# Kernel optimization log

Hardware: AMD Instinct MI355X
Metric: run time of the kernel (lower is better)

## Reference

```python
import jax, jax.numpy as jnp
import numpy as np
import math

B, S, D, H = 2, 2048, 768, 12
HD = D // H


def setup_inputs() -> dict:
    key = jax.random.key(0)
    ks = jax.random.split(key, 9)
    scale = 1.0 / math.sqrt(D)
    x = jax.random.normal(ks[0], (B, S, D), dtype=jnp.float32)
    # causal mask: True where attention is allowed (query i attends to key j<=i)
    mask = jnp.tril(jnp.ones((S, S), dtype=bool))[None, None]  # [1,1,S,S]
    wq = jax.random.normal(ks[1], (D, D), dtype=jnp.float32) * scale
    bq = jnp.zeros((D,), dtype=jnp.float32)
    wk = jax.random.normal(ks[2], (D, D), dtype=jnp.float32) * scale
    bk = jnp.zeros((D,), dtype=jnp.float32)
    wv = jax.random.normal(ks[3], (D, D), dtype=jnp.float32) * scale
    bv = jnp.zeros((D,), dtype=jnp.float32)
    wo = jax.random.normal(ks[4], (D, D), dtype=jnp.float32) * scale
    bo = jnp.zeros((D,), dtype=jnp.float32)
    return {"x": x, "mask": mask, "wq": wq, "bq": bq, "wk": wk, "bk": bk,
            "wv": wv, "bv": bv, "wo": wo, "bo": bo}


def reference(x, mask, wq, bq, wk, bk, wv, bv, wo, bo):
    b, s, d = x.shape
    # projections (flax Linear: y = x @ kernel + bias)
    q = (x @ wq + bq).reshape(b, s, H, HD).transpose(0, 2, 1, 3)  # [b,h,s,hd]
    k = (x @ wk + bk).reshape(b, s, H, HD).transpose(0, 2, 1, 3)
    v = (x @ wv + bv).reshape(b, s, H, HD).transpose(0, 2, 1, 3)
    scores = jnp.einsum('bhqd,bhkd->bhqk', q, k) / math.sqrt(HD)  # [b,h,s,s]
    scores = jnp.where(mask, scores, -jnp.inf)
    attn = jax.nn.softmax(scores, axis=-1)
    out = jnp.einsum('bhqk,bhkd->bhqd', attn, v)  # [b,h,s,hd]
    out = out.transpose(0, 2, 1, 3).reshape(b, s, d)
    return out @ wo + bo
```

## Files before the change

kernel.cpp:

```cpp
#include <hip/hip_runtime.h>
#include <math.h>

#define BATCH 2
#define SEQ   2048
#define DMODEL 768
#define NHEAD 12
#define HDIM  64

typedef unsigned short u16;
typedef __attribute__((ext_vector_type(8))) short bf16x8;
typedef __attribute__((ext_vector_type(4))) float f32x4;
typedef __attribute__((ext_vector_type(8))) unsigned short us8;
typedef __attribute__((ext_vector_type(4))) unsigned short us4;

__device__ __forceinline__ u16 f2bf(float f) {
    union { float f; unsigned u; } v; v.f = f;
    unsigned u = v.u;
    u += 0x7fff + ((u >> 16) & 1);
    return (u16)(u >> 16);
}

__device__ __forceinline__ u16 f2bf_trunc(float f) {
    union { float f; unsigned u; } v; v.f = f;
    return (u16)(v.u >> 16);
}

__device__ __forceinline__ float fexp2(float x) {
#if __has_builtin(__builtin_amdgcn_exp2f)
    return __builtin_amdgcn_exp2f(x);
#else
    return exp2f(x);
#endif
}

__device__ __forceinline__ void g2l16(const void* g, void* l) {
    __builtin_amdgcn_global_load_lds(
        (const __attribute__((address_space(1))) unsigned int*)g,
        (__attribute__((address_space(3))) unsigned int*)(unsigned int)(unsigned long long)(uintptr_t)l,
        16, 0, 0);
}

__device__ __forceinline__ void stage_rows(const u16* g, u16* lds, int nrows,
                                           int tid) {
    const int row = tid >> 2, col = (tid & 3) * 8;
    g2l16(g + (size_t)row * DMODEL + col, lds + tid * 8);
    if (nrows == 128) {
        g2l16(g + (size_t)(row + 64) * DMODEL + col, lds + 2048 + tid * 8);
    } else if (nrows == 96) {
        if (tid < 128)
            g2l16(g + (size_t)(row + 64) * DMODEL + col, lds + 2048 + tid * 8);
    }
}

__global__ __launch_bounds__(256) void prep(const float* __restrict__ x,
                                            const float* __restrict__ w0,
                                            const float* __restrict__ w1,
                                            const float* __restrict__ w2,
                                            const float* __restrict__ w3,
                                            u16* __restrict__ xb,
                                            u16* __restrict__ Wt_all) {
    __shared__ float t[32][33];
    const int bid = blockIdx.x;
    if (bid < 3072) {
        int i = bid * 256 + threadIdx.x;
        float4 v = ((const float4*)x)[i];
        us4 o;
        o.x = f2bf(v.x); o.y = f2bf(v.y); o.z = f2bf(v.z); o.w = f2bf(v.w);
        *(us4*)&xb[(size_t)i * 4] = o;
    } else {
        const int wid = bid - 3072;
        const int z  = wid / 576;
        const int rr = wid % 576;
        const int by = rr / 24, bx = rr % 24;
        const float* W = z == 0 ? w0 : z == 1 ? w1 : z == 2 ? w2 : w3;
        u16* Wt = Wt_all + (size_t)z * DMODEL * DMODEL;

        int tx = threadIdx.x & 31, ty = threadIdx.x >> 5;
        int xg = bx * 32 + tx;
        #pragma unroll
        for (int j = 0; j < 32; j += 8)
            t[ty + j][tx] = W[(size_t)(by * 32 + ty + j) * DMODEL + xg];
        __syncthreads();
        int x2 = by * 32 + tx;
        #pragma unroll
        for (int j = 0; j < 32; j += 8)
            Wt[(size_t)(bx * 32 + ty + j) * DMODEL + x2] = f2bf(t[tx][ty + j]);
    }
}

__global__ __launch_bounds__(256) void gemm_qkv(
    const u16* __restrict__ xb, const u16* __restrict__ WtQK,
    const u16* __restrict__ WtV,
    const float* __restrict__ bq, const float* __restrict__ bk,
    const float* __restrict__ bv,
    u16* __restrict__ QK, u16* __restrict__ Vt) {

    __shared__ __align__(16) u16 As[128 * 32];
    __shared__ __align__(16) u16 Bs[128 * 32];

    const int tid  = threadIdx.x;
    const int lane = tid & 63;
    const int w    = tid >> 6;
    const int quad = lane >> 4, l16 = lane & 15;
    const int wm   = w >> 1, wn = w & 1;
    const int b    = blockIdx.x;

    if (b < 512) {
        const int m0 = (b >> 4) * 128;
        const int n0 = (b & 15) * 96;
        f32x4 acc[4][3] = {};
        for (int k0 = 0; k0 < DMODEL; k0 += 32) {
            stage_rows(xb   + (size_t)m0 * DMODEL + k0, As, 128, tid);
            stage_rows(WtQK + (size_t)n0 * DMODEL + k0, Bs,  96, tid);
            __syncthreads();
            bf16x8 af[4], bfr[3];
            #pragma unroll
            for (int i = 0; i < 4; ++i)
                af[i] = *(const bf16x8*)&As[(wm * 64 + i * 16 + l16) * 32 + quad * 8];
            #pragma unroll
            for (int j = 0; j < 3; ++j)
                bfr[j] = *(const bf16x8*)&Bs[(wn * 48 + j * 16 + l16) * 32 + quad * 8];
            #pragma unroll
            for (int i = 0; i < 4; ++i)
                #pragma unroll
                for (int j = 0; j < 3; ++j)
                    acc[i][j] = __builtin_amdgcn_mfma_f32_16x16x32_bf16(af[i], bfr[j], acc[i][j], 0, 0, 0);
            __syncthreads();
        }
        const size_t n_elem = (size_t)BATCH * SEQ * DMODEL;
        #pragma unroll
        for (int j = 0; j < 3; ++j) {
            const int n     = n0 + wn * 48 + j * 16 + l16;
            const int which = n / 768;
            const int nn    = n - which * 768;
            const float bias  = (which == 0 ? bq : bk)[nn];
            const float scale = (which == 0) ? 0.18033688011112043f : 1.0f;
            const int h = nn >> 6, hd = nn & 63;
            u16* outw = QK + (size_t)which * n_elem;
            #pragma unroll
            for (int i = 0; i < 4; ++i) {
                const int mbase = m0 + wm * 64 + i * 16 + quad * 4;
                #pragma unroll
                for (int r = 0; r < 4; ++r) {
                    const int m  = mbase + r;
                    const int b_ = m >> 11, s_ = m & 2047;
                    outw[(size_t)((b_ * NHEAD + h) * SEQ + s_) * HDIM + hd] =
                        f2bf((acc[i][j][r] + bias) * scale);
                }
            }
        }
    } else {
        const int vj = b - 512;
        const int m0 = (vj & 7) * 96;
        const int n0 = (vj >> 3) * 128;
        f32x4 acc[3][4] = {};
        for (int k0 = 0; k0 < DMODEL; k0 += 32) {
            stage_rows(WtV + (size_t)m0 * DMODEL + k0, As,  96, tid);
            stage_rows(xb  + (size_t)n0 * DMODEL + k0, Bs, 128, tid);
            __syncthreads();
            bf16x8 af[3], bfr[4];
            #pragma unroll
            for (int i = 0; i < 3; ++i)
                af[i] = *(const bf16x8*)&As[(wm * 48 + i * 16 + l16) * 32 + quad * 8];
            #pragma unroll
            for (int j = 0; j < 4; ++j)
                bfr[j] = *(const bf16x8*)&Bs[(wn * 64 + j * 16 + l16) * 32 + quad * 8];
            #pragma unroll
            for (int i = 0; i < 3; ++i)
                #pragma unroll
                for (int j = 0; j < 4; ++j)
                    acc[i][j] = __builtin_amdgcn_mfma_f32_16x16x32_bf16(af[i], bfr[j], acc[i][j], 0, 0, 0);
            __syncthreads();
        }
        #pragma unroll
        for (int i = 0; i < 3; ++i) {
            const int rbase = m0 + wm * 48 + i * 16 + quad * 4;
            #pragma unroll
            for (int r = 0; r < 4; ++r) {
                const int row_g = rbase + r;
                const float bias = bv[row_g];
                const int h = row_g >> 6, hd = row_g & 63;
                #pragma unroll
                for (int j = 0; j < 4; ++j) {
                    const int col_g = n0 + wn * 64 + j * 16 + l16;
                    const int b_ = col_g >> 11, s_ = col_g & 2047;
                    Vt[(size_t)((b_ * NHEAD + h) * HDIM + hd) * SEQ + s_] =
                        f2bf(acc[i][j][r] + bias);
                }
            }
        }
    }
}

__global__ __launch_bounds__(256) void gemm_out(
    const u16* __restrict__ Ag, const u16* __restrict__ Bt,
    const float* __restrict__ bo, float* __restrict__ out) {

    __shared__ __align__(16) u16 As[64 * 32];
    __shared__ __align__(16) u16 Bs[64 * 32];

    const int tid  = threadIdx.x;
    const int lane = tid & 63;
    const int w    = tid >> 6;
    const int quad = lane >> 4, l16 = lane & 15;
    const int wm   = w >> 1, wn = w & 1;
    const int m0 = blockIdx.x * 64, n0 = blockIdx.y * 64;

    const int rowA = tid >> 2;
    const int kch  = (tid & 3) * 8;

    f32x4 acc[2][2] = {};

    for (int k0 = 0; k0 < DMODEL; k0 += 32) {
        g2l16(Ag + (size_t)(m0 + rowA) * DMODEL + k0 + kch, As + tid * 8);
        g2l16(Bt + (size_t)(n0 + rowA) * DMODEL + k0 + kch, Bs + tid * 8);
        __syncthreads();

        bf16x8 af[2], bfr[2];
        #pragma unroll
        for (int i = 0; i < 2; ++i)
            af[i] = *(const bf16x8*)&As[(wm * 32 + i * 16 + l16) * 32 + quad * 8];
        #pragma unroll
        for (int j = 0; j < 2; ++j)
            bfr[j] = *(const bf16x8*)&Bs[(wn * 32 + j * 16 + l16) * 32 + quad * 8];
        #pragma unroll
        for (int i = 0; i < 2; ++i)
            #pragma unroll
            for (int j = 0; j < 2; ++j)
                acc[i][j] = __builtin_amdgcn_mfma_f32_16x16x32_bf16(af[i], bfr[j], acc[i][j], 0, 0, 0);
        __syncthreads();
    }

    #pragma unroll
    for (int i = 0; i < 2; ++i) {
        const int mbase = m0 + wm * 32 + i * 16 + quad * 4;
        #pragma unroll
        for (int r = 0; r < 4; ++r) {
            const int m = mbase + r;
            #pragma unroll
            for (int j = 0; j < 2; ++j) {
                const int n = n0 + wn * 32 + j * 16 + l16;
                out[(size_t)m * DMODEL + n] = acc[i][j][r] + bo[n];
            }
        }
    }
}

__global__ __launch_bounds__(256) void flash_attn_mfma(
    const u16* __restrict__ Q, const u16* __restrict__ K,
    const u16* __restrict__ Vt, u16* __restrict__ A) {

    __shared__ __align__(16) u16 Kl[3][64 * 64];
    __shared__ __align__(16) u16 Vl[3][64 * 64];
    __shared__ __align__(16) u16 Pl[4][16 * 72];

    const int tid  = threadIdx.x;
    const int lane = tid & 63;
    const int w    = tid >> 6;
    const int quad = lane >> 4;
    const int l16  = lane & 15;

    const int sid = 767 - (int)blockIdx.x;
    const int j   = sid / 24;
    const int bh  = sid - j * 24;
    const int tc  = j + 1;

    const size_t base = (size_t)bh * SEQ * HDIM;
    const u16* Qg = Q + base;
    const u16* Kg = K + base;
    const u16* Vg = Vt + base;

    const int wrow0 = j * 64 + w * 16;
    const int qrow  = wrow0 + quad * 4;

    bf16x8 qf0 = *(const bf16x8*)&Qg[(size_t)(wrow0 + l16) * 64 + quad * 8];
    bf16x8 qf1 = *(const bf16x8*)&Qg[(size_t)(wrow0 + l16) * 64 + quad * 8 + 32];

    f32x4 o[4] = {};
    float l_acc[4] = {0.f, 0.f, 0.f, 0.f};

    const int pwbase = 2 * quad + (l16 >> 3);
    const int prd0   = (quad + 2 * (l16 >> 2)) & 7;
    u16* Pw = Pl[w];
    const u16* pr0 = &Pw[l16 * 72 + prd0 * 8];
    const u16* pr1 = &Pw[l16 * 72 + (prd0 ^ 4) * 8];

    const int ch0 = tid, ch1 = tid + 256;
    const int r0 = ch0 >> 3, lc0 = (ch0 & 7) ^ (r0 & 7);
    const int r1 = ch1 >> 3, lc1 = (ch1 & 7) ^ (r1 & 7);
    const u16* kp0 = Kg + (size_t)r0 * 64 + lc0 * 8;
    const u16* kp1 = Kg + (size_t)r1 * 64 + lc1 * 8;
    const u16* vp0 = Vg + (size_t)r0 * SEQ + lc0 * 8;
    const u16* vp1 = Vg + (size_t)r1 * SEQ + lc1 * 8;

    auto STAGE = [&](int buf) {
        g2l16(kp0, &Kl[buf][ch0 * 8]);
        g2l16(kp1, &Kl[buf][ch1 * 8]);
        g2l16(vp0, &Vl[buf][ch0 * 8]);
        g2l16(vp1, &Vl[buf][ch1 * 8]);
        kp0 += 64 * 64; kp1 += 64 * 64;
        vp0 += 64;      vp1 += 64;
    };

    STAGE(0);
    if (tc > 1) STAGE(1);

    int cur = 0, nb = 2;
    for (int t = 0; t < tc; ++t) {
        if (t + 1 < tc) asm volatile("s_waitcnt vmcnt(4)" ::: "memory");
        else            asm volatile("s_waitcnt vmcnt(0)" ::: "memory");
        __builtin_amdgcn_s_barrier();
        if (t + 2 < tc) { STAGE(nb); nb = (nb == 2) ? 0 : nb + 1; }

        const int j0 = t * 64;
        const u16* Kc = Kl[cur];
        const u16* Vc = Vl[cur];

        f32x4 s[4];
        __builtin_amdgcn_s_setprio(1);
        #pragma unroll
        for (int c4 = 0; c4 < 4; ++c4) {
            const int krow = c4 * 16 + l16;
            const int pc = (quad ^ (krow & 7)) * 8;
            bf16x8 kf0 = *(const bf16x8*)&Kc[krow * 64 + pc];
            bf16x8 kf1 = *(const bf16x8*)&Kc[krow * 64 + (pc ^ 32)];
            f32x4 a2 = {};
            a2 = __builtin_amdgcn_mfma_f32_16x16x32_bf16(qf0, kf0, a2, 0, 0, 0);
            a2 = __builtin_amdgcn_mfma_f32_16x16x32_bf16(qf1, kf1, a2, 0, 0, 0);
            s[c4] = a2;
        }
        __builtin_amdgcn_s_setprio(0);

        if (t == tc - 1) {
            #pragma unroll
            for (int c4 = 0; c4 < 4; ++c4) {
                const int jg = j0 + c4 * 16 + l16;
                #pragma unroll
                for (int r = 0; r < 4; ++r)
                    if (jg > qrow + r) s[c4][r] = -INFINITY;
            }
        }

        #pragma unroll
        for (int c4 = 0; c4 < 4; ++c4)
            #pragma unroll
            for (int r = 0; r < 4; ++r)
                s[c4][r] = fexp2(s[c4][r]);
        #pragma unroll
        for (int r = 0; r < 4; ++r)
            l_acc[r] += (s[0][r] + s[1][r]) + (s[2][r] + s[3][r]);

        #pragma unroll
        for (int c4 = 0; c4 < 4; ++c4) {
            const int pc = ((2 * c4 + pwbase) & 7) * 8 + (l16 & 7);
            #pragma unroll
            for (int r = 0; r < 4; ++r)
                Pw[(quad * 4 + r) * 72 + pc] = f2bf_trunc(s[c4][r]);
        }
        bf16x8 pf0 = *(const bf16x8*)pr0;
        bf16x8 pf1 = *(const bf16x8*)pr1;

        __builtin_amdgcn_s_setprio(1);
        #pragma unroll
        for (int c2 = 0; c2 < 4; ++c2) {
            const int vrow = c2 * 16 + l16;
            const int vc = (quad ^ (vrow & 7)) * 8;
            bf16x8 vf0 = *(const bf16x8*)&Vc[vrow * 64 + vc];
            bf16x8 vf1 = *(const bf16x8*)&Vc[vrow * 64 + (vc ^ 32)];
            o[c2] = __builtin_amdgcn_mfma_f32_16x16x32_bf16(pf0, vf0, o[c2], 0, 0, 0);
            o[c2] = __builtin_amdgcn_mfma_f32_16x16x32_bf16(pf1, vf1, o[c2], 0, 0, 0);
        }
        __builtin_amdgcn_s_setprio(0);

        cur = (cur == 2) ? 0 : cur + 1;
    }

    #pragma unroll
    for (int off = 1; off < 16; off <<= 1)
        #pragma unroll
        for (int r = 0; r < 4; ++r)
            l_acc[r] += __shfl_xor(l_acc[r], off);

    const int b = bh / NHEAD, h = bh % NHEAD;
    #pragma unroll
    for (int r = 0; r < 4; ++r) {
        float inv = 1.0f / l_acc[r];
        int sg = qrow + r;
        u16* dst = A + ((size_t)(b * SEQ + sg)) * DMODEL + h * HDIM;
        #pragma unroll
        for (int c2 = 0; c2 < 4; ++c2)
            dst[c2 * 16 + l16] = f2bf(o[c2][r] * inv);
    }
}

extern "C" void kernel_launch(void* const* d_in, const int* in_sizes, int n_in,
                              void* d_out, int out_size, void* d_ws, size_t ws_size,
                              hipStream_t stream) {
    const float* x  = (const float*)d_in[0];
    const float* wq = (const float*)d_in[2];
    const float* bq = (const float*)d_in[3];
    const float* wk = (const float*)d_in[4];
    const float* bk = (const float*)d_in[5];
    const float* wv = (const float*)d_in[6];
    const float* bv = (const float*)d_in[7];
    const float* wo = (const float*)d_in[8];
    const float* bo = (const float*)d_in[9];
    float* out = (float*)d_out;

    const size_t n_elem = (size_t)BATCH * SEQ * DMODEL;
    const size_t w_elem = (size_t)DMODEL * DMODEL;

    u16* xb     = (u16*)d_ws;
    u16* Wt_all = xb + n_elem;
    u16* Qw     = Wt_all + 4 * w_elem;
    u16* Vtw    = Qw + 2 * n_elem;
    u16* Aw     = Vtw + n_elem;

    dim3 blk(256);

    prep<<<dim3(3072 + 2304), blk, 0, stream>>>(x, wq, wk, wv, wo, xb, Wt_all);

    gemm_qkv<<<dim3(768), blk, 0, stream>>>(xb, Wt_all, Wt_all + 2 * w_elem,
                                            bq, bk, bv, Qw, Vtw);

    flash_attn_mfma<<<dim3(768), blk, 0, stream>>>(Qw, Qw + n_elem, Vtw, Aw);

    gemm_out<<<dim3(64, 12), blk, 0, stream>>>(Aw, Wt_all + 3 * w_elem, bo, out);
}
```

Before: 162.3 us.

## Restructure flash attention around 32x32 MFMA with register-resident P and 2 waves

Rewrites the attention kernel to use 32x32x16 bf16 MFMAs with 2 waves per block, each covering 32 query rows. S is computed transposed (K as A operand), so P can be converted with v_cvt_pk_bf16_f32 and rearranged with v_permlane32_swap instead of a round trip through LDS. The upper 32-key half is skipped on diagonal tiles, and the output is staged through LDS for vectorized 16-byte stores. This removes the P LDS traffic and the scalar stores, at the cost of fewer waves per block, more staging work per thread and higher register pressure from f32x16 accumulators.

```diff
diff --git a/kernel.cpp b/kernel.cpp
--- a/kernel.cpp
+++ b/kernel.cpp
@@ -10,6 +10,7 @@
 typedef unsigned short u16;
 typedef __attribute__((ext_vector_type(8))) short bf16x8;
 typedef __attribute__((ext_vector_type(4))) float f32x4;
+typedef __attribute__((ext_vector_type(16))) float f32x16;
 typedef __attribute__((ext_vector_type(8))) unsigned short us8;
 typedef __attribute__((ext_vector_type(4))) unsigned short us4;
 
@@ -18,11 +19,6 @@
     unsigned u = v.u;
     u += 0x7fff + ((u >> 16) & 1);
     return (u16)(u >> 16);
-}
-
-__device__ __forceinline__ u16 f2bf_trunc(float f) {
-    union { float f; unsigned u; } v; v.f = f;
-    return (u16)(v.u >> 16);
 }
 
 __device__ __forceinline__ float fexp2(float x) {
@@ -246,19 +242,18 @@
     }
 }
 
-__global__ __launch_bounds__(256) void flash_attn_mfma(
+__global__ __launch_bounds__(128) void flash_attn_mfma(
     const u16* __restrict__ Q, const u16* __restrict__ K,
     const u16* __restrict__ Vt, u16* __restrict__ A) {
 
     __shared__ __align__(16) u16 Kl[3][64 * 64];
     __shared__ __align__(16) u16 Vl[3][64 * 64];
-    __shared__ __align__(16) u16 Pl[4][16 * 72];
 
     const int tid  = threadIdx.x;
     const int lane = tid & 63;
     const int w    = tid >> 6;
-    const int quad = lane >> 4;
-    const int l16  = lane & 15;
+    const int l32  = lane & 31;
+    const int hi   = lane >> 5;
 
     const int sid = 767 - (int)blockIdx.x;
     const int j   = sid / 24;
@@ -270,127 +265,145 @@
     const u16* Kg = K + base;
     const u16* Vg = Vt + base;
 
-    const int wrow0 = j * 64 + w * 16;
-    const int qrow  = wrow0 + quad * 4;
-
-    bf16x8 qf0 = *(const bf16x8*)&Qg[(size_t)(wrow0 + l16) * 64 + quad * 8];
-    bf16x8 qf1 = *(const bf16x8*)&Qg[(size_t)(wrow0 + l16) * 64 + quad * 8 + 32];
-
-    f32x4 o[4] = {};
-    float l_acc[4] = {0.f, 0.f, 0.f, 0.f};
-
-    const int pwbase = 2 * quad + (l16 >> 3);
-    const int prd0   = (quad + 2 * (l16 >> 2)) & 7;
-    u16* Pw = Pl[w];
-    const u16* pr0 = &Pw[l16 * 72 + prd0 * 8];
-    const u16* pr1 = &Pw[l16 * 72 + (prd0 ^ 4) * 8];
-
-    const int ch0 = tid, ch1 = tid + 256;
-    const int r0 = ch0 >> 3, lc0 = (ch0 & 7) ^ (r0 & 7);
-    const int r1 = ch1 >> 3, lc1 = (ch1 & 7) ^ (r1 & 7);
-    const u16* kp0 = Kg + (size_t)r0 * 64 + lc0 * 8;
-    const u16* kp1 = Kg + (size_t)r1 * 64 + lc1 * 8;
-    const u16* vp0 = Vg + (size_t)r0 * SEQ + lc0 * 8;
-    const u16* vp1 = Vg + (size_t)r1 * SEQ + lc1 * 8;
+    const int wq0   = j * 64 + w * 32;
+    const int wlast = wq0 + 31;
+    const int qg    = wq0 + l32;
+
+    bf16x8 qf[4];
+    #pragma unroll
+    for (int c = 0; c < 4; ++c)
+        qf[c] = *(const bf16x8*)&Qg[(size_t)qg * 64 + 16 * c + 8 * hi];
+
+    f32x16 o0 = {}, o1 = {};
+    float l_acc = 0.f;
+
+    const u16* kp[4]; const u16* vp[4];
+    #pragma unroll
+    for (int i = 0; i < 4; ++i) {
+        const int ch = tid + i * 128;
+        const int r  = ch >> 3, lc = (ch & 7) ^ (r & 7);
+        kp[i] = Kg + (size_t)r * 64 + lc * 8;
+        vp[i] = Vg + (size_t)r * SEQ + lc * 8;
+    }
 
     auto STAGE = [&](int buf) {
-        g2l16(kp0, &Kl[buf][ch0 * 8]);
-        g2l16(kp1, &Kl[buf][ch1 * 8]);
-        g2l16(vp0, &Vl[buf][ch0 * 8]);
-        g2l16(vp1, &Vl[buf][ch1 * 8]);
-        kp0 += 64 * 64; kp1 += 64 * 64;
-        vp0 += 64;      vp1 += 64;
+        #pragma unroll
+        for (int i = 0; i < 4; ++i) {
+            const int ch = tid + i * 128;
+            g2l16(kp[i], &Kl[buf][ch * 8]);
+            g2l16(vp[i], &Vl[buf][ch * 8]);
+            kp[i] += 64 * 64;
+            vp[i] += 64;
+        }
     };
 
     STAGE(0);
     if (tc > 1) STAGE(1);
 
     int cur = 0, nb = 2;
+    const int cx = l32 & 7;
     for (int t = 0; t < tc; ++t) {
-        if (t + 1 < tc) asm volatile("s_waitcnt vmcnt(4)" ::: "memory");
+        if (t + 1 < tc) asm volatile("s_waitcnt vmcnt(8)" ::: "memory");
         else            asm volatile("s_waitcnt vmcnt(0)" ::: "memory");
         __builtin_amdgcn_s_barrier();
         if (t + 2 < tc) { STAGE(nb); nb = (nb == 2) ? 0 : nb + 1; }
 
-        const int j0 = t * 64;
         const u16* Kc = Kl[cur];
         const u16* Vc = Vl[cur];
-
-        f32x4 s[4];
+        const int j0 = t * 64;
+        const bool do1 = (j0 + 32 <= wlast);
+
+        f32x16 s0 = {}, s1 = {};
         __builtin_amdgcn_s_setprio(1);
         #pragma unroll
-        for (int c4 = 0; c4 < 4; ++c4) {
-            const int krow = c4 * 16 + l16;
-            const int pc = (quad ^ (krow & 7)) * 8;
-            bf16x8 kf0 = *(const bf16x8*)&Kc[krow * 64 + pc];
-            bf16x8 kf1 = *(const bf16x8*)&Kc[krow * 64 + (pc ^ 32)];
-            f32x4 a2 = {};
-            a2 = __builtin_amdgcn_mfma_f32_16x16x32_bf16(qf0, kf0, a2, 0, 0, 0);
-            a2 = __builtin_amdgcn_mfma_f32_16x16x32_bf16(qf1, kf1, a2, 0, 0, 0);
-            s[c4] = a2;
+        for (int c = 0; c < 4; ++c) {
+            bf16x8 kf = *(const bf16x8*)&Kc[l32 * 64 + (((2 * c + hi) ^ cx) * 8)];
+            s0 = __builtin_amdgcn_mfma_f32_32x32x16_bf16(kf, qf[c], s0, 0, 0, 0);
+        }
+        if (do1) {
+            #pragma unroll
+            for (int c = 0; c < 4; ++c) {
+                bf16x8 kf = *(const bf16x8*)&Kc[(32 + l32) * 64 + (((2 * c + hi) ^ cx) * 8)];
+                s1 = __builtin_amdgcn_mfma_f32_32x32x16_bf16(kf, qf[c], s1, 0, 0, 0);
+            }
         }
         __builtin_amdgcn_s_setprio(0);
 
         if (t == tc - 1) {
             #pragma unroll
-            for (int c4 = 0; c4 < 4; ++c4) {
-                const int jg = j0 + c4 * 16 + l16;
+            for (int r = 0; r < 16; ++r) {
+                const int key = j0 + (r & 3) + 8 * (r >> 2) + 4 * hi;
+                if (key > qg) s0[r] = -INFINITY;
+            }
+            if (do1) {
                 #pragma unroll
-                for (int r = 0; r < 4; ++r)
-                    if (jg > qrow + r) s[c4][r] = -INFINITY;
-            }
-        }
-
-        #pragma unroll
-        for (int c4 = 0; c4 < 4; ++c4)
-            #pragma unroll
-            for (int r = 0; r < 4; ++r)
-                s[c4][r] = fexp2(s[c4][r]);
-        #pragma unroll
-        for (int r = 0; r < 4; ++r)
-            l_acc[r] += (s[0][r] + s[1][r]) + (s[2][r] + s[3][r]);
-
-        #pragma unroll
-        for (int c4 = 0; c4 < 4; ++c4) {
-            const int pc = ((2 * c4 + pwbase) & 7) * 8 + (l16 & 7);
-            #pragma unroll
-            for (int r = 0; r < 4; ++r)
-                Pw[(quad * 4 + r) * 72 + pc] = f2bf_trunc(s[c4][r]);
-        }
-        bf16x8 pf0 = *(const bf16x8*)pr0;
-        bf16x8 pf1 = *(const bf16x8*)pr1;
+                for (int r = 0; r < 16; ++r) {
+                    const int key = j0 + 32 + (r & 3) + 8 * (r >> 2) + 4 * hi;
+                    if (key > qg) s1[r] = -INFINITY;
+                }
+            }
+        }
+
+        #pragma unroll
+        for (int r = 0; r < 16; ++r) s0[r] = fexp2(s0[r]);
+        if (do1) {
+            #pragma unroll
+            for (int r = 0; r < 16; ++r) s1[r] = fexp2(s1[r]);
+        }
+        float ps = 0.f;
+        #pragma unroll
+        for (int r = 0; r < 16; ++r) ps += s0[r] + s1[r];
+        l_acc += ps;
+
+        bf16x8 pa[4];
+        #pragma unroll
+        for (int kw = 0; kw < 4; ++kw) {
+            const f32x16& sv = (kw < 2) ? s0 : s1;
+            const int m0i = 2 * (kw & 1);
+            unsigned a0l, a0h, a1l, a1h;
+            asm("v_cvt_pk_bf16_f32 %0, %1, %2" : "=v"(a0l) : "v"(sv[4 * m0i + 0]), "v"(sv[4 * m0i + 1]));
+            asm("v_cvt_pk_bf16_f32 %0, %1, %2" : "=v"(a0h) : "v"(sv[4 * m0i + 2]), "v"(sv[4 * m0i + 3]));
+            asm("v_cvt_pk_bf16_f32 %0, %1, %2" : "=v"(a1l) : "v"(sv[4 * (m0i + 1) + 0]), "v"(sv[4 * (m0i + 1) + 1]));
+            asm("v_cvt_pk_bf16_f32 %0, %1, %2" : "=v"(a1h) : "v"(sv[4 * (m0i + 1) + 2]), "v"(sv[4 * (m0i + 1) + 3]));
+            asm("v_permlane32_swap_b32 %0, %1" : "+v"(a0l), "+v"(a1l));
+            asm("v_permlane32_swap_b32 %0, %1" : "+v"(a0h), "+v"(a1h));
+            union { unsigned u[4]; bf16x8 v; } pu;
+            pu.u[0] = a0l; pu.u[1] = a0h; pu.u[2] = a1l; pu.u[3] = a1h;
+            pa[kw] = pu.v;
+        }
 
         __builtin_amdgcn_s_setprio(1);
         #pragma unroll
-        for (int c2 = 0; c2 < 4; ++c2) {
-            const int vrow = c2 * 16 + l16;
-            const int vc = (quad ^ (vrow & 7)) * 8;
-            bf16x8 vf0 = *(const bf16x8*)&Vc[vrow * 64 + vc];
-            bf16x8 vf1 = *(const bf16x8*)&Vc[vrow * 64 + (vc ^ 32)];
-            o[c2] = __builtin_amdgcn_mfma_f32_16x16x32_bf16(pf0, vf0, o[c2], 0, 0, 0);
-            o[c2] = __builtin_amdgcn_mfma_f32_16x16x32_bf16(pf1, vf1, o[c2], 0, 0, 0);
+        for (int kw = 0; kw < 4; ++kw) {
+            const int pc = ((2 * kw + hi) ^ cx) * 8;
+            bf16x8 vf0 = *(const bf16x8*)&Vc[l32 * 64 + pc];
+            bf16x8 vf1 = *(const bf16x8*)&Vc[(32 + l32) * 64 + pc];
+            o0 = __builtin_amdgcn_mfma_f32_32x32x16_bf16(vf0, pa[kw], o0, 0, 0, 0);
+            o1 = __builtin_amdgcn_mfma_f32_32x32x16_bf16(vf1, pa[kw], o1, 0, 0, 0);
         }
         __builtin_amdgcn_s_setprio(0);
 
         cur = (cur == 2) ? 0 : cur + 1;
     }
 
+    __syncthreads();
+
+    const float tot = l_acc + __shfl_xor(l_acc, 32);
+    const float inv = 1.0f / tot;
+
+    u16* Ot = ((u16*)Kl) + w * 2304;
     #pragma unroll
-    for (int off = 1; off < 16; off <<= 1)
-        #pragma unroll
-        for (int r = 0; r < 4; ++r)
-            l_acc[r] += __shfl_xor(l_acc[r], off);
-
-    const int b = bh / NHEAD, h = bh % NHEAD;
+    for (int r = 0; r < 16; ++r) {
+        const int d = (r & 3) + 8 * (r >> 2) + 4 * hi;
+        Ot[l32 * 72 + d]      = f2bf(o0[r] * inv);
+        Ot[l32 * 72 + 32 + d] = f2bf(o1[r] * inv);
+    }
+    const int row = lane >> 1, d0 = (lane & 1) * 32;
+    const int b_ = bh / NHEAD, h_ = bh % NHEAD;
+    u16* dst = A + ((size_t)(b_ * SEQ + wq0 + row)) * DMODEL + h_ * HDIM + d0;
     #pragma unroll
-    for (int r = 0; r < 4; ++r) {
-        float inv = 1.0f / l_acc[r];
-        int sg = qrow + r;
-        u16* dst = A + ((size_t)(b * SEQ + sg)) * DMODEL + h * HDIM;
-        #pragma unroll
-        for (int c2 = 0; c2 < 4; ++c2)
-            dst[c2 * 16 + l16] = f2bf(o[c2][r] * inv);
-    }
+    for (int k2 = 0; k2 < 4; ++k2)
+        *(us8*)&dst[k2 * 8] = *(const us8*)&Ot[row * 72 + d0 + k2 * 8];
 }
 
 extern "C" void kernel_launch(void* const* d_in, const int* in_sizes, int n_in,
@@ -423,7 +436,7 @@
     gemm_qkv<<<dim3(768), blk, 0, stream>>>(xb, Wt_all, Wt_all + 2 * w_elem,
                                             bq, bk, bv, Qw, Vtw);
 
-    flash_attn_mfma<<<dim3(768), blk, 0, stream>>>(Qw, Qw + n_elem, Vtw, Aw);
+    flash_attn_mfma<<<dim3(768), dim3(128), 0, stream>>>(Qw, Qw + n_elem, Vtw, Aw);
 
     gemm_out<<<dim3(64, 12), blk, 0, stream>>>(Aw, Wt_all + 3 * w_elem, bo, out);
 }
```

New measurement: 171.7 us. 1.06x slower.
